# Kernel tuning notes

Measured on AMD Instinct MI355X. Metric: run time of the kernel, lower is better.

The kernel has to match this reference:

```python
import jax, jax.numpy as jnp
import numpy as np

# Model dims (Gemma-class)
B, T, HID = 1, 3072, 2048
H, KH, D = 16, 8, 128          # q heads, kv heads, head_dim
WIN = 1024                     # sliding window
EPS = 1e-6
SEQ = 1536                     # two packed sequences of length 1536


def _rms(x, w):
    # torch nn.RMSNorm: x * rsqrt(mean(x^2) + eps) [* weight]
    var = jnp.mean(x * x, axis=-1, keepdims=True)
    y = x * jax.lax.rsqrt(var + EPS)
    return y if w is None else y * w


def _rotate_half(x):
    x1, x2 = jnp.split(x, 2, axis=-1)
    return jnp.concatenate([-x2, x1], axis=-1)


def _rope(x, cos, sin):
    # x: [B,T,h,D]; cos/sin: [B,T,rd] -> unsqueeze head dim (matches cos.unsqueeze(2))
    c = cos[:, :, None, :]
    s = sin[:, :, None, :]
    rd = cos.shape[-1]
    xr, xp = x[..., :rd], x[..., rd:]
    xr = xr * c + _rotate_half(xr) * s
    return jnp.concatenate([xr, xp], axis=-1)


def _build_mask(cu_seqlens):
    # causal & within sliding window & same packed sequence (matches _sliding_mask)
    idx = jnp.arange(T)
    seg = jnp.searchsorted(cu_seqlens, idx, side='right') - 1
    i = idx[:, None]
    j = idx[None, :]
    return (i >= j) & ((i - j) < WIN) & (seg[:, None] == seg[None, :])


def _attn_layer(x, wq, qn, k, v, wo, cos, sin, mask):
    # x: [B,T,HID]; k,v: [T,KH,D] (possibly shared from an earlier layer)
    q = _rope(_rms((x @ wq).reshape(B, T, H, D), qn), cos, sin).reshape(T, H, D)
    rep = H // k.shape[1]
    kk = jnp.repeat(k, rep, axis=1)   # GQA: repeat_interleave over head dim
    vv = jnp.repeat(v, rep, axis=1)
    s = jnp.einsum('qhd,khd->hqk', q, kk)          # scale = 1.0 (as in source)
    s = jnp.where(mask, s, jnp.asarray(-1e30, s.dtype))
    p = jax.nn.softmax(s, axis=-1)
    o = jnp.einsum('hqk,khd->qhd', p, vv).reshape(B, T, H * D)
    return o @ wo


def setup_inputs() -> dict:
    key = jax.random.key(0)
    ks = jax.random.split(key, 10)
    hidden_states = jax.random.normal(ks[0], (B, T, HID), jnp.float32)
    # RoPE tables with per-packed-sequence position resets
    pos = jnp.concatenate([jnp.arange(SEQ), jnp.arange(SEQ)]).astype(jnp.float32)
    inv = 1.0 / (10000.0 ** (jnp.arange(0, D, 2, dtype=jnp.float32) / D))
    fr = pos[:, None] * inv[None, :]
    emb = jnp.concatenate([fr, fr], axis=-1)     # [T, D]
    cos = jnp.cos(emb)[None]                     # [1, T, D]
    sin = jnp.sin(emb)[None]
    w = lambda k, sh: 0.02 * jax.random.normal(k, sh, jnp.float32)
    return {
        'hidden_states': hidden_states,
        'cos': cos, 'sin': sin,
        'wq0': w(ks[1], (HID, H * D)), 'wk0': w(ks[2], (HID, KH * D)),
        'wv0': w(ks[3], (HID, KH * D)), 'wo0': w(ks[4], (H * D, HID)),
        'qn0': 1.0 + 0.01 * jax.random.normal(ks[5], (D,), jnp.float32),
        'kn0': 1.0 + 0.01 * jax.random.normal(ks[6], (D,), jnp.float32),
        'wq1': w(ks[7], (HID, H * D)), 'wo1': w(ks[8], (H * D, HID)),
        'qn1': 1.0 + 0.01 * jax.random.normal(ks[9], (D,), jnp.float32),
        'cu_seqlens': jnp.array([0, SEQ, T], dtype=jnp.int32),
    }


def reference(hidden_states, cos, sin, wq0, wk0, wv0, wo0, qn0, kn0, wq1, wo1, qn1, cu_seqlens):
    mask = _build_mask(cu_seqlens)
    # Layer 0: source layer -> computes and stores K/V
    k = _rope(_rms((hidden_states @ wk0).reshape(B, T, KH, D), kn0), cos, sin).reshape(T, KH, D)
    v = _rms((hidden_states @ wv0).reshape(B, T, KH, D), None).reshape(T, KH, D)
    out0 = _attn_layer(hidden_states, wq0, qn0, k, v, wo0, cos, sin, mask)
    # Layer 1: KV-shared layer -> reuses layer 0's K/V (skips k/v projections)
    out1 = _attn_layer(out0, wq1, qn1, k, v, wo1, cos, sin, mask)
    return out1
```

## Files before the change

kernel.cpp:

```cpp
#include <hip/hip_runtime.h>
#include <hip/hip_bf16.h>

#define T_TOK 3072
#define HIDDEN 2048
#define NHQ 16
#define NHKV 8
#define DH 128
#define WINDOW 1024

typedef __attribute__((ext_vector_type(4))) float f32x4;
typedef __attribute__((ext_vector_type(8))) short bf16x8;
typedef __attribute__((ext_vector_type(8))) unsigned short ushort8;
typedef __attribute__((ext_vector_type(4))) unsigned short ushort4v;

__device__ __forceinline__ unsigned short f2bf(float f) {
  union { float fv; unsigned u; } v; v.fv = f;
  unsigned r = v.u + 0x7fffu + ((v.u >> 16) & 1u);
  return (unsigned short)(r >> 16);
}
__device__ __forceinline__ float bf2f(unsigned short h) {
  union { unsigned u; float f; } v; v.u = ((unsigned)h) << 16;
  return v.f;
}
__device__ __forceinline__ void split2(float f, unsigned short& hi, unsigned short& lo) {
  hi = f2bf(f);
  lo = f2bf(f - bf2f(hi));
}

__global__ __launch_bounds__(256) void cvt_split(const float* __restrict__ x,
                                                 unsigned short* __restrict__ yh,
                                                 unsigned short* __restrict__ yl, int n) {
  int i = (blockIdx.x * 256 + threadIdx.x) * 4;
  if (i >= n) return;
  f32x4 v = *(const f32x4*)(x + i);
  ushort4v oh, ol;
#pragma unroll
  for (int j = 0; j < 4; ++j) {
    unsigned short h, l;
    split2(v[j], h, l);
    oh[j] = h; ol[j] = l;
  }
  *(ushort4v*)(yh + i) = oh;
  *(ushort4v*)(yl + i) = ol;
}

__global__ __launch_bounds__(256) void transpose_w_split(const float* __restrict__ W,
                                                         unsigned short* __restrict__ Wth,
                                                         unsigned short* __restrict__ Wtl,
                                                         int K, int N) {
  __shared__ float tile[32][33];
  int bn = blockIdx.x * 32, bk = blockIdx.y * 32;
  int tx = threadIdx.x & 31, ty = threadIdx.x >> 5;
#pragma unroll
  for (int i = 0; i < 4; ++i)
    tile[ty + i * 8][tx] = W[(size_t)(bk + ty + i * 8) * N + bn + tx];
  __syncthreads();
#pragma unroll
  for (int i = 0; i < 4; ++i) {
    unsigned short h, l;
    split2(tile[tx][ty + i * 8], h, l);
    Wth[(size_t)(bn + ty + i * 8) * K + bk + tx] = h;
    if (Wtl) Wtl[(size_t)(bn + ty + i * 8) * K + bk + tx] = l;
  }
}

__global__ __launch_bounds__(256) void transpose_u16(const unsigned short* __restrict__ src,
                                                     unsigned short* __restrict__ dst,
                                                     int R, int C) {
  __shared__ unsigned short tile[32][33];
  int bc = blockIdx.x * 32, br = blockIdx.y * 32;
  int tx = threadIdx.x & 31, ty = threadIdx.x >> 5;
#pragma unroll
  for (int i = 0; i < 4; ++i)
    tile[ty + i * 8][tx] = src[(size_t)(br + ty + i * 8) * C + bc + tx];
  __syncthreads();
#pragma unroll
  for (int i = 0; i < 4; ++i)
    dst[(size_t)(bc + ty + i * 8) * R + br + tx] = tile[tx][ty + i * 8];
}

template <int OUT>
__global__ __launch_bounds__(256) void gemm3(const unsigned short* __restrict__ Ah,
                                             const unsigned short* __restrict__ Al,
                                             const unsigned short* __restrict__ Bh,
                                             const unsigned short* __restrict__ Bl,
                                             float* __restrict__ Cf,
                                             unsigned short* __restrict__ Ch,
                                             unsigned short* __restrict__ Cl,
                                             int M, int N, int K) {
  __shared__ unsigned short ah_lds[128 * 32];
  __shared__ unsigned short al_lds[128 * 32];
  __shared__ unsigned short bh_lds[128 * 32];
  __shared__ unsigned short bl_lds[128 * 32];
  const int tid = threadIdx.x, lane = tid & 63, wave = tid >> 6;
  const int wr = (wave >> 1) * 64, wc = (wave & 1) * 64;
  const int g = lane >> 4, r16 = lane & 15;
  int nwg = gridDim.x * gridDim.y;
  int id = blockIdx.y * gridDim.x + blockIdx.x;
  int nid = (id & 7) * (nwg >> 3) + (id >> 3);
  const int bm = nid % gridDim.x, bn = nid / gridDim.x;
  f32x4 acc[4][4];
#pragma unroll
  for (int i = 0; i < 4; ++i)
#pragma unroll
    for (int j = 0; j < 4; ++j) acc[i][j] = (f32x4){0.f, 0.f, 0.f, 0.f};

  const unsigned short* AhB = Ah + (size_t)bm * 128 * K;
  const unsigned short* AlB = Al + (size_t)bm * 128 * K;
  const unsigned short* BhB = Bh + (size_t)bn * 128 * K;
  const unsigned short* BlB = Bl + (size_t)bn * 128 * K;

  for (int kt = 0; kt < K; kt += 32) {
    __syncthreads();
#pragma unroll
    for (int c = 0; c < 2; ++c) {
      size_t goff = (size_t)(wave * 32 + c * 16 + (lane >> 2)) * K + kt + (lane & 3) * 8;
      int loff = (wave * 2 + c) * 512;
      __builtin_amdgcn_global_load_lds(
          (const __attribute__((address_space(1))) unsigned int*)(AhB + goff),
          (__attribute__((address_space(3))) unsigned int*)(ah_lds + loff), 16, 0, 0);
      __builtin_amdgcn_global_load_lds(
          (const __attribute__((address_space(1))) unsigned int*)(AlB + goff),
          (__attribute__((address_space(3))) unsigned int*)(al_lds + loff), 16, 0, 0);
      __builtin_amdgcn_global_load_lds(
          (const __attribute__((address_space(1))) unsigned int*)(BhB + goff),
          (__attribute__((address_space(3))) unsigned int*)(bh_lds + loff), 16, 0, 0);
      __builtin_amdgcn_global_load_lds(
          (const __attribute__((address_space(1))) unsigned int*)(BlB + goff),
          (__attribute__((address_space(3))) unsigned int*)(bl_lds + loff), 16, 0, 0);
    }
    __syncthreads();
    bf16x8 ahf[4], alf[4], bhf[4], blf[4];
#pragma unroll
    for (int i = 0; i < 4; ++i) {
      ahf[i] = *(const bf16x8*)&ah_lds[(wr + i * 16 + r16) * 32 + g * 8];
      alf[i] = *(const bf16x8*)&al_lds[(wr + i * 16 + r16) * 32 + g * 8];
      bhf[i] = *(const bf16x8*)&bh_lds[(wc + i * 16 + r16) * 32 + g * 8];
      blf[i] = *(const bf16x8*)&bl_lds[(wc + i * 16 + r16) * 32 + g * 8];
    }
#pragma unroll
    for (int i = 0; i < 4; ++i)
#pragma unroll
      for (int j = 0; j < 4; ++j) {
        acc[i][j] = __builtin_amdgcn_mfma_f32_16x16x32_bf16(ahf[i], bhf[j], acc[i][j], 0, 0, 0);
        acc[i][j] = __builtin_amdgcn_mfma_f32_16x16x32_bf16(ahf[i], blf[j], acc[i][j], 0, 0, 0);
        acc[i][j] = __builtin_amdgcn_mfma_f32_16x16x32_bf16(alf[i], bhf[j], acc[i][j], 0, 0, 0);
      }
  }

#pragma unroll
  for (int i = 0; i < 4; ++i) {
    int row = bm * 128 + wr + i * 16 + g * 4;
#pragma unroll
    for (int j = 0; j < 4; ++j) {
      int col = bn * 128 + wc + j * 16 + r16;
#pragma unroll
      for (int r = 0; r < 4; ++r) {
        if (OUT == 0) {
          Cf[(size_t)(row + r) * N + col] = acc[i][j][r];
        } else {
          unsigned short h, l;
          split2(acc[i][j][r], h, l);
          Ch[(size_t)(row + r) * N + col] = h;
          Cl[(size_t)(row + r) * N + col] = l;
        }
      }
    }
  }
}

__global__ __launch_bounds__(256) void gemm1(const unsigned short* __restrict__ Ah,
                                             const unsigned short* __restrict__ Bh,
                                             float* __restrict__ Cf,
                                             int M, int N, int K) {
  __shared__ unsigned short ah_lds[128 * 32];
  __shared__ unsigned short bh_lds[128 * 32];
  const int tid = threadIdx.x, lane = tid & 63, wave = tid >> 6;
  const int wr = (wave >> 1) * 64, wc = (wave & 1) * 64;
  const int g = lane >> 4, r16 = lane & 15;
  int nwg = gridDim.x * gridDim.y;
  int id = blockIdx.y * gridDim.x + blockIdx.x;
  int nid = (id & 7) * (nwg >> 3) + (id >> 3);
  const int bm = nid % gridDim.x, bn = nid / gridDim.x;
  f32x4 acc[4][4];
#pragma unroll
  for (int i = 0; i < 4; ++i)
#pragma unroll
    for (int j = 0; j < 4; ++j) acc[i][j] = (f32x4){0.f, 0.f, 0.f, 0.f};

  const unsigned short* AhB = Ah + (size_t)bm * 128 * K;
  const unsigned short* BhB = Bh + (size_t)bn * 128 * K;

  for (int kt = 0; kt < K; kt += 32) {
    __syncthreads();
#pragma unroll
    for (int c = 0; c < 2; ++c) {
      size_t goff = (size_t)(wave * 32 + c * 16 + (lane >> 2)) * K + kt + (lane & 3) * 8;
      int loff = (wave * 2 + c) * 512;
      __builtin_amdgcn_global_load_lds(
          (const __attribute__((address_space(1))) unsigned int*)(AhB + goff),
          (__attribute__((address_space(3))) unsigned int*)(ah_lds + loff), 16, 0, 0);
      __builtin_amdgcn_global_load_lds(
          (const __attribute__((address_space(1))) unsigned int*)(BhB + goff),
          (__attribute__((address_space(3))) unsigned int*)(bh_lds + loff), 16, 0, 0);
    }
    __syncthreads();
    bf16x8 ahf[4], bhf[4];
#pragma unroll
    for (int i = 0; i < 4; ++i) {
      ahf[i] = *(const bf16x8*)&ah_lds[(wr + i * 16 + r16) * 32 + g * 8];
      bhf[i] = *(const bf16x8*)&bh_lds[(wc + i * 16 + r16) * 32 + g * 8];
    }
#pragma unroll
    for (int i = 0; i < 4; ++i)
#pragma unroll
      for (int j = 0; j < 4; ++j)
        acc[i][j] = __builtin_amdgcn_mfma_f32_16x16x32_bf16(ahf[i], bhf[j], acc[i][j], 0, 0, 0);
  }

#pragma unroll
  for (int i = 0; i < 4; ++i) {
    int row = bm * 128 + wr + i * 16 + g * 4;
#pragma unroll
    for (int j = 0; j < 4; ++j) {
      int col = bn * 128 + wc + j * 16 + r16;
#pragma unroll
      for (int r = 0; r < 4; ++r)
        Cf[(size_t)(row + r) * N + col] = acc[i][j][r];
    }
  }
}

__global__ __launch_bounds__(256) void rms_rope_split(const float* __restrict__ X,
                                                      const float* __restrict__ w,
                                                      const float* __restrict__ cosp,
                                                      const float* __restrict__ sinp,
                                                      unsigned short* __restrict__ outh,
                                                      unsigned short* __restrict__ outl,
                                                      int NH, int doRope) {
  int row = blockIdx.x * 4 + (threadIdx.x >> 6);
  int lane = threadIdx.x & 63;
  const float* x = X + (size_t)row * DH;
  float x1 = x[lane], x2 = x[lane + 64];
  float ss = x1 * x1 + x2 * x2;
#pragma unroll
  for (int m = 1; m < 64; m <<= 1) ss += __shfl_xor(ss, m, 64);
  float inv = rsqrtf(ss * (1.0f / 128.0f) + 1e-6f);
  float y1 = x1 * inv, y2 = x2 * inv;
  if (w) { y1 *= w[lane]; y2 *= w[lane + 64]; }
  if (doRope) {
    int t = row / NH;
    float c1 = cosp[t * DH + lane], s1 = sinp[t * DH + lane];
    float c2 = cosp[t * DH + lane + 64], s2 = sinp[t * DH + lane + 64];
    float o1 = y1 * c1 - y2 * s1;
    float o2 = y2 * c2 + y1 * s2;
    y1 = o1; y2 = o2;
  }
  unsigned short h, l;
  split2(y1, h, l);
  outh[(size_t)row * DH + lane] = h;
  if (outl) outl[(size_t)row * DH + lane] = l;
  split2(y2, h, l);
  outh[(size_t)row * DH + lane + 64] = h;
  if (outl) outl[(size_t)row * DH + lane + 64] = l;
}

template <int WRITE_LO>
__global__ __launch_bounds__(256) void attn3(const unsigned short* __restrict__ Qh,
                                             const unsigned short* __restrict__ Ql,
                                             const unsigned short* __restrict__ Kh,
                                             const unsigned short* __restrict__ Kl,
                                             const unsigned short* __restrict__ Vth,
                                             unsigned short* __restrict__ Oh,
                                             unsigned short* __restrict__ Ol,
                                             const int* __restrict__ cu, int ncu) {
  __shared__ unsigned short kh_lds[32][136];
  __shared__ unsigned short kl_lds[32][136];
  __shared__ unsigned short vh_lds[144][40];
  __shared__ unsigned short ph_lds[4][16][40];

  int id = blockIdx.y * gridDim.x + blockIdx.x;
  int nid = (id & 7) * 96 + (id >> 3);
  const int qt = nid % 48, h = nid / 48;
  const int qbase = qt * 64;
  const int kvh = h >> 1;
  const int tid = threadIdx.x, lane = tid & 63, wave = tid >> 6;
  const int g = lane >> 4, r16 = lane & 15;

  for (int i = tid; i < 16 * 40; i += 256) {
    int rr = i / 40, cc = i % 40;
    vh_lds[128 + rr][cc] = (rr == 0) ? (unsigned short)0x3F80 : (unsigned short)0;
  }

  bf16x8 aqh[4], aql[4];
  {
    const size_t qoff = ((size_t)(qbase + wave * 16 + r16) * NHQ + h) * DH;
#pragma unroll
    for (int ks = 0; ks < 4; ++ks) {
      aqh[ks] = *(const bf16x8*)(Qh + qoff + ks * 32 + g * 8);
      aql[ks] = *(const bf16x8*)(Ql + qoff + ks * 32 + g * 8);
    }
  }

  int ssr[4];
#pragma unroll
  for (int r = 0; r < 4; ++r) {
    int q_r = qbase + wave * 16 + g * 4 + r;
    int s = 0;
    for (int i = 1; i < ncu; ++i) { int v = cu[i]; if (v <= q_r) s = v; }
    ssr[r] = s;
  }
  int ss_base = 0;
  for (int i = 1; i < ncu; ++i) { int v = cu[i]; if (v <= qbase) ss_base = v; }

  float m_r[4] = {-1e30f, -1e30f, -1e30f, -1e30f};
  f32x4 oacc[8];
#pragma unroll
  for (int db = 0; db < 8; ++db) oacc[db] = (f32x4){0.f, 0.f, 0.f, 0.f};
  f32x4 oaccL = (f32x4){0.f, 0.f, 0.f, 0.f};

  int lo = qbase - WINDOW + 1;
  if (lo < ss_base) lo = ss_base;
  if (lo < 0) lo = 0;
  int kt0 = lo & ~31;
  int ktend = qbase + 63;

  const int krow = tid >> 3, kcol = (tid & 7) * 16;
  const int vd = tid >> 1, vhalf = (tid & 1) * 16;
  const int qmin = qbase + wave * 16;

  ushort8 rkh0, rkh1, rkl0, rkl1, rvh0, rvh1;
  auto loadTile = [&](int kt) {
    size_t goff = ((size_t)(kt + krow) * NHKV + kvh) * DH + kcol;
    rkh0 = *(const ushort8*)(Kh + goff);
    rkh1 = *(const ushort8*)(Kh + goff + 8);
    rkl0 = *(const ushort8*)(Kl + goff);
    rkl1 = *(const ushort8*)(Kl + goff + 8);
    size_t voff = ((size_t)kvh * DH + vd) * T_TOK + kt + vhalf;
    rvh0 = *(const ushort8*)(Vth + voff);
    rvh1 = *(const ushort8*)(Vth + voff + 8);
  };
  auto writeTile = [&]() {
    *(ushort8*)&kh_lds[krow][kcol] = rkh0;
    *(ushort8*)&kh_lds[krow][kcol + 8] = rkh1;
    *(ushort8*)&kl_lds[krow][kcol] = rkl0;
    *(ushort8*)&kl_lds[krow][kcol + 8] = rkl1;
    *(ushort8*)&vh_lds[vd][vhalf] = rvh0;
    *(ushort8*)&vh_lds[vd][vhalf + 8] = rvh1;
  };

  loadTile(kt0);
  writeTile();
  __syncthreads();

  for (int kt = kt0; kt <= ktend; kt += 32) {
    const bool hasNext = (kt + 32 <= ktend);
    if (hasNext) loadTile(kt + 32);

    f32x4 s0 = (f32x4){0.f, 0.f, 0.f, 0.f}, s1 = (f32x4){0.f, 0.f, 0.f, 0.f};
#pragma unroll
    for (int ks = 0; ks < 4; ++ks) {
      bf16x8 bh0 = *(const bf16x8*)&kh_lds[r16][ks * 32 + g * 8];
      bf16x8 bh1 = *(const bf16x8*)&kh_lds[16 + r16][ks * 32 + g * 8];
      bf16x8 bl0 = *(const bf16x8*)&kl_lds[r16][ks * 32 + g * 8];
      bf16x8 bl1 = *(const bf16x8*)&kl_lds[16 + r16][ks * 32 + g * 8];
      s0 = __builtin_amdgcn_mfma_f32_16x16x32_bf16(aqh[ks], bh0, s0, 0, 0, 0);
      s0 = __builtin_amdgcn_mfma_f32_16x16x32_bf16(aqh[ks], bl0, s0, 0, 0, 0);
      s0 = __builtin_amdgcn_mfma_f32_16x16x32_bf16(aql[ks], bh0, s0, 0, 0, 0);
      s1 = __builtin_amdgcn_mfma_f32_16x16x32_bf16(aqh[ks], bh1, s1, 0, 0, 0);
      s1 = __builtin_amdgcn_mfma_f32_16x16x32_bf16(aqh[ks], bl1, s1, 0, 0, 0);
      s1 = __builtin_amdgcn_mfma_f32_16x16x32_bf16(aql[ks], bh1, s1, 0, 0, 0);
    }

    float sv0_[4], sv1_[4], mt_[4];
    bool ok0_[4], ok1_[4];
    bool interior = (kt + 31 <= qmin) && (kt >= qmin + 16 - WINDOW) &&
                    __all(kt >= ssr[3]);
    if (interior) {
#pragma unroll
      for (int r = 0; r < 4; ++r) {
        ok0_[r] = ok1_[r] = true;
        sv0_[r] = s0[r]; sv1_[r] = s1[r];
      }
    } else {
#pragma unroll
      for (int r = 0; r < 4; ++r) {
        int q_r = qmin + g * 4 + r;
        int k0 = kt + r16, k1 = k0 + 16;
        ok0_[r] = (k0 <= q_r) && (k0 > q_r - WINDOW) && (k0 >= ssr[r]);
        ok1_[r] = (k1 <= q_r) && (k1 > q_r - WINDOW) && (k1 >= ssr[r]);
        sv0_[r] = ok0_[r] ? s0[r] : -1e30f;
        sv1_[r] = ok1_[r] ? s1[r] : -1e30f;
      }
    }
#pragma unroll
    for (int r = 0; r < 4; ++r) {
      float mt = fmaxf(sv0_[r], sv1_[r]);
#pragma unroll
      for (int mm = 1; mm < 16; mm <<= 1) mt = fmaxf(mt, __shfl_xor(mt, mm, 64));
      mt_[r] = mt;
    }
    float grow = fmaxf(fmaxf(mt_[0] - m_r[0], mt_[1] - m_r[1]),
                       fmaxf(mt_[2] - m_r[2], mt_[3] - m_r[3]));
    if (!__all(grow <= 8.0f)) {
#pragma unroll
      for (int r = 0; r < 4; ++r) {
        float mnew = fmaxf(m_r[r], mt_[r]);
        float alpha = __expf(m_r[r] - mnew);
        m_r[r] = mnew;
#pragma unroll
        for (int db = 0; db < 8; ++db) oacc[db][r] *= alpha;
        oaccL[r] *= alpha;
      }
    }
#pragma unroll
    for (int r = 0; r < 4; ++r) {
      float p0 = ok0_[r] ? __expf(sv0_[r] - m_r[r]) : 0.f;
      float p1 = ok1_[r] ? __expf(sv1_[r] - m_r[r]) : 0.f;
      ph_lds[wave][g * 4 + r][r16] = f2bf(p0);
      ph_lds[wave][g * 4 + r][16 + r16] = f2bf(p1);
    }

    bf16x8 pah = *(const bf16x8*)&ph_lds[wave][r16][g * 8];
#pragma unroll
    for (int db = 0; db < 8; ++db) {
      bf16x8 vfh = *(const bf16x8*)&vh_lds[db * 16 + r16][g * 8];
      oacc[db] = __builtin_amdgcn_mfma_f32_16x16x32_bf16(pah, vfh, oacc[db], 0, 0, 0);
    }
    {
      bf16x8 vfo = *(const bf16x8*)&vh_lds[128 + r16][g * 8];
      oaccL = __builtin_amdgcn_mfma_f32_16x16x32_bf16(pah, vfo, oaccL, 0, 0, 0);
    }

    __syncthreads();
    if (hasNext) writeTile();
    __syncthreads();
  }

#pragma unroll
  for (int r = 0; r < 4; ++r) {
    int q_r = qbase + wave * 16 + g * 4 + r;
    float lsum = __shfl(oaccL[r], lane & 48, 64);
    float invl = 1.f / lsum;
#pragma unroll
    for (int db = 0; db < 8; ++db) {
      float ov = oacc[db][r] * invl;
      unsigned short hh, ll;
      split2(ov, hh, ll);
      Oh[(size_t)q_r * (NHQ * DH) + h * DH + db * 16 + r16] = hh;
      if (WRITE_LO) Ol[(size_t)q_r * (NHQ * DH) + h * DH + db * 16 + r16] = ll;
    }
  }
}

extern "C" void kernel_launch(void* const* d_in, const int* in_sizes, int n_in,
                              void* d_out, int out_size, void* d_ws, size_t ws_size,
                              hipStream_t stream) {
  const float* hidden = (const float*)d_in[0];
  const float* cosp   = (const float*)d_in[1];
  const float* sinp   = (const float*)d_in[2];
  const float* wq0    = (const float*)d_in[3];
  const float* wk0    = (const float*)d_in[4];
  const float* wv0    = (const float*)d_in[5];
  const float* wo0    = (const float*)d_in[6];
  const float* qn0    = (const float*)d_in[7];
  const float* kn0    = (const float*)d_in[8];
  const float* wq1    = (const float*)d_in[9];
  const float* wo1    = (const float*)d_in[10];
  const float* qn1    = (const float*)d_in[11];
  const int*   cu     = (const int*)d_in[12];
  int ncu = in_sizes[12];

  char* p = (char*)d_ws;
  auto alloc = [&](size_t bytes) { char* r = p; p += (bytes + 255) & ~255ull; return r; };
  float*          c32  = (float*)alloc((size_t)T_TOK * HIDDEN * 4);
  unsigned short* xh   = (unsigned short*)alloc((size_t)T_TOK * HIDDEN * 2);
  unsigned short* xl   = (unsigned short*)alloc((size_t)T_TOK * HIDDEN * 2);
  unsigned short* wth  = (unsigned short*)alloc((size_t)HIDDEN * HIDDEN * 2);
  unsigned short* wtl  = (unsigned short*)alloc((size_t)HIDDEN * HIDDEN * 2);
  unsigned short* qh   = (unsigned short*)alloc((size_t)T_TOK * NHQ * DH * 2);
  unsigned short* ql   = (unsigned short*)alloc((size_t)T_TOK * NHQ * DH * 2);
  unsigned short* kh   = (unsigned short*)alloc((size_t)T_TOK * NHKV * DH * 2);
  unsigned short* kl   = (unsigned short*)alloc((size_t)T_TOK * NHKV * DH * 2);
  unsigned short* vh   = (unsigned short*)alloc((size_t)T_TOK * NHKV * DH * 2);
  unsigned short* vth  = (unsigned short*)alloc((size_t)T_TOK * NHKV * DH * 2);
  unsigned short* x1h  = (unsigned short*)alloc((size_t)T_TOK * HIDDEN * 2);
  unsigned short* x1l  = (unsigned short*)alloc((size_t)T_TOK * HIDDEN * 2);
  (void)ws_size; (void)n_in; (void)out_size;

  const int nX = T_TOK * HIDDEN;
  const int KVN = NHKV * DH;

  cvt_split<<<nX / 1024, 256, 0, stream>>>(hidden, xh, xl, nX);

  transpose_w_split<<<dim3(HIDDEN / 32, HIDDEN / 32), 256, 0, stream>>>(wq0, wth, wtl, HIDDEN, HIDDEN);
  gemm3<0><<<dim3(T_TOK / 128, HIDDEN / 128), 256, 0, stream>>>(xh, xl, wth, wtl, c32, nullptr, nullptr, T_TOK, HIDDEN, HIDDEN);
  rms_rope_split<<<T_TOK * NHQ / 4, 256, 0, stream>>>(c32, qn0, cosp, sinp, qh, ql, NHQ, 1);

  transpose_w_split<<<dim3(KVN / 32, HIDDEN / 32), 256, 0, stream>>>(wk0, wth, wtl, HIDDEN, KVN);
  gemm3<0><<<dim3(T_TOK / 128, KVN / 128), 256, 0, stream>>>(xh, xl, wth, wtl, c32, nullptr, nullptr, T_TOK, KVN, HIDDEN);
  rms_rope_split<<<T_TOK * NHKV / 4, 256, 0, stream>>>(c32, kn0, cosp, sinp, kh, kl, NHKV, 1);

  transpose_w_split<<<dim3(KVN / 32, HIDDEN / 32), 256, 0, stream>>>(wv0, wth, nullptr, HIDDEN, KVN);
  gemm1<<<dim3(T_TOK / 128, KVN / 128), 256, 0, stream>>>(xh, wth, c32, T_TOK, KVN, HIDDEN);
  rms_rope_split<<<T_TOK * NHKV / 4, 256, 0, stream>>>(c32, nullptr, cosp, sinp, vh, nullptr, NHKV, 0);

  transpose_u16<<<dim3(KVN / 32, T_TOK / 32), 256, 0, stream>>>(vh, vth, T_TOK, KVN);

  attn3<1><<<dim3(T_TOK / 64, NHQ), 256, 0, stream>>>(qh, ql, kh, kl, vth, xh, xl, cu, ncu);

  transpose_w_split<<<dim3(HIDDEN / 32, HIDDEN / 32), 256, 0, stream>>>(wo0, wth, wtl, HIDDEN, HIDDEN);
  gemm3<2><<<dim3(T_TOK / 128, HIDDEN / 128), 256, 0, stream>>>(xh, xl, wth, wtl, nullptr, x1h, x1l, T_TOK, HIDDEN, HIDDEN);

  transpose_w_split<<<dim3(HIDDEN / 32, HIDDEN / 32), 256, 0, stream>>>(wq1, wth, wtl, HIDDEN, HIDDEN);
  gemm3<0><<<dim3(T_TOK / 128, HIDDEN / 128), 256, 0, stream>>>(x1h, x1l, wth, wtl, c32, nullptr, nullptr, T_TOK, HIDDEN, HIDDEN);
  rms_rope_split<<<T_TOK * NHQ / 4, 256, 0, stream>>>(c32, qn1, cosp, sinp, qh, ql, NHQ, 1);

  attn3<0><<<dim3(T_TOK / 64, NHQ), 256, 0, stream>>>(qh, ql, kh, kl, vth, xh, nullptr, cu, ncu);

  transpose_w_split<<<dim3(HIDDEN / 32, HIDDEN / 32), 256, 0, stream>>>(wo1, wth, nullptr, HIDDEN, HIDDEN);
  gemm1<<<dim3(T_TOK / 128, HIDDEN / 128), 256, 0, stream>>>(xh, wth, (float*)d_out, T_TOK, HIDDEN, HIDDEN);
}
```

Measured before the change: 747.1 us.

## Load K/V MFMA operands directly from global memory instead of LDS staging

```diff
diff --git a/kernel.cpp b/kernel.cpp
--- a/kernel.cpp
+++ b/kernel.cpp
@@ -274,9 +274,6 @@
                                              unsigned short* __restrict__ Oh,
                                              unsigned short* __restrict__ Ol,
                                              const int* __restrict__ cu, int ncu) {
-  __shared__ unsigned short kh_lds[32][136];
-  __shared__ unsigned short kl_lds[32][136];
-  __shared__ unsigned short vh_lds[144][40];
   __shared__ unsigned short ph_lds[4][16][40];
 
   int id = blockIdx.y * gridDim.x + blockIdx.x;
@@ -287,11 +284,6 @@
   const int tid = threadIdx.x, lane = tid & 63, wave = tid >> 6;
   const int g = lane >> 4, r16 = lane & 15;
 
-  for (int i = tid; i < 16 * 40; i += 256) {
-    int rr = i / 40, cc = i % 40;
-    vh_lds[128 + rr][cc] = (rr == 0) ? (unsigned short)0x3F80 : (unsigned short)0;
-  }
-
   bf16x8 aqh[4], aql[4];
   {
     const size_t qoff = ((size_t)(qbase + wave * 16 + r16) * NHQ + h) * DH;
@@ -325,51 +317,41 @@
   int kt0 = lo & ~31;
   int ktend = qbase + 63;
 
-  const int krow = tid >> 3, kcol = (tid & 7) * 16;
-  const int vd = tid >> 1, vhalf = (tid & 1) * 16;
   const int qmin = qbase + wave * 16;
 
-  ushort8 rkh0, rkh1, rkl0, rkl1, rvh0, rvh1;
-  auto loadTile = [&](int kt) {
-    size_t goff = ((size_t)(kt + krow) * NHKV + kvh) * DH + kcol;
-    rkh0 = *(const ushort8*)(Kh + goff);
-    rkh1 = *(const ushort8*)(Kh + goff + 8);
-    rkl0 = *(const ushort8*)(Kl + goff);
-    rkl1 = *(const ushort8*)(Kl + goff + 8);
-    size_t voff = ((size_t)kvh * DH + vd) * T_TOK + kt + vhalf;
-    rvh0 = *(const ushort8*)(Vth + voff);
-    rvh1 = *(const ushort8*)(Vth + voff + 8);
-  };
-  auto writeTile = [&]() {
-    *(ushort8*)&kh_lds[krow][kcol] = rkh0;
-    *(ushort8*)&kh_lds[krow][kcol + 8] = rkh1;
-    *(ushort8*)&kl_lds[krow][kcol] = rkl0;
-    *(ushort8*)&kl_lds[krow][kcol + 8] = rkl1;
-    *(ushort8*)&vh_lds[vd][vhalf] = rvh0;
-    *(ushort8*)&vh_lds[vd][vhalf + 8] = rvh1;
-  };
-
-  loadTile(kt0);
-  writeTile();
-  __syncthreads();
+  bf16x8 vfo;
+#pragma unroll
+  for (int j = 0; j < 8; ++j) vfo[j] = (r16 == 0) ? (short)0x3F80 : (short)0;
+
+  const size_t kstr = (size_t)NHKV * DH;
+  const unsigned short* kh0 = Kh + ((size_t)r16 * NHKV + kvh) * DH + g * 8;
+  const unsigned short* kh1 = Kh + ((size_t)(r16 + 16) * NHKV + kvh) * DH + g * 8;
+  const unsigned short* kl0 = Kl + ((size_t)r16 * NHKV + kvh) * DH + g * 8;
+  const unsigned short* kl1 = Kl + ((size_t)(r16 + 16) * NHKV + kvh) * DH + g * 8;
+  const unsigned short* vt0 = Vth + ((size_t)(kvh * DH + r16)) * T_TOK + g * 8;
 
   for (int kt = kt0; kt <= ktend; kt += 32) {
-    const bool hasNext = (kt + 32 <= ktend);
-    if (hasNext) loadTile(kt + 32);
-
     f32x4 s0 = (f32x4){0.f, 0.f, 0.f, 0.f}, s1 = (f32x4){0.f, 0.f, 0.f, 0.f};
-#pragma unroll
-    for (int ks = 0; ks < 4; ++ks) {
-      bf16x8 bh0 = *(const bf16x8*)&kh_lds[r16][ks * 32 + g * 8];
-      bf16x8 bh1 = *(const bf16x8*)&kh_lds[16 + r16][ks * 32 + g * 8];
-      bf16x8 bl0 = *(const bf16x8*)&kl_lds[r16][ks * 32 + g * 8];
-      bf16x8 bl1 = *(const bf16x8*)&kl_lds[16 + r16][ks * 32 + g * 8];
-      s0 = __builtin_amdgcn_mfma_f32_16x16x32_bf16(aqh[ks], bh0, s0, 0, 0, 0);
-      s0 = __builtin_amdgcn_mfma_f32_16x16x32_bf16(aqh[ks], bl0, s0, 0, 0, 0);
-      s0 = __builtin_amdgcn_mfma_f32_16x16x32_bf16(aql[ks], bh0, s0, 0, 0, 0);
-      s1 = __builtin_amdgcn_mfma_f32_16x16x32_bf16(aqh[ks], bh1, s1, 0, 0, 0);
-      s1 = __builtin_amdgcn_mfma_f32_16x16x32_bf16(aqh[ks], bl1, s1, 0, 0, 0);
-      s1 = __builtin_amdgcn_mfma_f32_16x16x32_bf16(aql[ks], bh1, s1, 0, 0, 0);
+    {
+      const unsigned short* p0 = kh0 + (size_t)kt * kstr;
+      const unsigned short* p1 = kh1 + (size_t)kt * kstr;
+      const unsigned short* q0 = kl0 + (size_t)kt * kstr;
+      const unsigned short* q1 = kl1 + (size_t)kt * kstr;
+      __builtin_amdgcn_s_setprio(1);
+#pragma unroll
+      for (int ks = 0; ks < 4; ++ks) {
+        bf16x8 bh0 = *(const bf16x8*)(p0 + ks * 32);
+        bf16x8 bh1 = *(const bf16x8*)(p1 + ks * 32);
+        bf16x8 bl0 = *(const bf16x8*)(q0 + ks * 32);
+        bf16x8 bl1 = *(const bf16x8*)(q1 + ks * 32);
+        s0 = __builtin_amdgcn_mfma_f32_16x16x32_bf16(aqh[ks], bh0, s0, 0, 0, 0);
+        s0 = __builtin_amdgcn_mfma_f32_16x16x32_bf16(aqh[ks], bl0, s0, 0, 0, 0);
+        s0 = __builtin_amdgcn_mfma_f32_16x16x32_bf16(aql[ks], bh0, s0, 0, 0, 0);
+        s1 = __builtin_amdgcn_mfma_f32_16x16x32_bf16(aqh[ks], bh1, s1, 0, 0, 0);
+        s1 = __builtin_amdgcn_mfma_f32_16x16x32_bf16(aqh[ks], bl1, s1, 0, 0, 0);
+        s1 = __builtin_amdgcn_mfma_f32_16x16x32_bf16(aql[ks], bh1, s1, 0, 0, 0);
+      }
+      __builtin_amdgcn_s_setprio(0);
     }
 
     float sv0_[4], sv1_[4], mt_[4];
@@ -415,26 +397,24 @@
     }
 #pragma unroll
     for (int r = 0; r < 4; ++r) {
-      float p0 = ok0_[r] ? __expf(sv0_[r] - m_r[r]) : 0.f;
-      float p1 = ok1_[r] ? __expf(sv1_[r] - m_r[r]) : 0.f;
-      ph_lds[wave][g * 4 + r][r16] = f2bf(p0);
-      ph_lds[wave][g * 4 + r][16 + r16] = f2bf(p1);
+      float p0v = ok0_[r] ? __expf(sv0_[r] - m_r[r]) : 0.f;
+      float p1v = ok1_[r] ? __expf(sv1_[r] - m_r[r]) : 0.f;
+      ph_lds[wave][g * 4 + r][r16] = f2bf(p0v);
+      ph_lds[wave][g * 4 + r][16 + r16] = f2bf(p1v);
     }
 
     bf16x8 pah = *(const bf16x8*)&ph_lds[wave][r16][g * 8];
-#pragma unroll
-    for (int db = 0; db < 8; ++db) {
-      bf16x8 vfh = *(const bf16x8*)&vh_lds[db * 16 + r16][g * 8];
-      oacc[db] = __builtin_amdgcn_mfma_f32_16x16x32_bf16(pah, vfh, oacc[db], 0, 0, 0);
-    }
     {
-      bf16x8 vfo = *(const bf16x8*)&vh_lds[128 + r16][g * 8];
+      const unsigned short* vb = vt0 + kt;
+      __builtin_amdgcn_s_setprio(1);
+#pragma unroll
+      for (int db = 0; db < 8; ++db) {
+        bf16x8 vfh = *(const bf16x8*)(vb + (size_t)db * 16 * T_TOK);
+        oacc[db] = __builtin_amdgcn_mfma_f32_16x16x32_bf16(pah, vfh, oacc[db], 0, 0, 0);
+      }
       oaccL = __builtin_amdgcn_mfma_f32_16x16x32_bf16(pah, vfo, oaccL, 0, 0, 0);
-    }
-
-    __syncthreads();
-    if (hasNext) writeTile();
-    __syncthreads();
+      __builtin_amdgcn_s_setprio(0);
+    }
   }
 
 #pragma unroll
```

Result: slower. 979.3 us (+31.1%).

## Halve GEMM M-tile to 64 and fuse K/V projections into one GEMM

Applied to the files above, without the earlier changes.

```diff
diff --git a/kernel.cpp b/kernel.cpp
--- a/kernel.cpp
+++ b/kernel.cpp
@@ -80,48 +80,52 @@
 }
 
 template <int OUT>
-__global__ __launch_bounds__(256) void gemm3(const unsigned short* __restrict__ Ah,
-                                             const unsigned short* __restrict__ Al,
-                                             const unsigned short* __restrict__ Bh,
-                                             const unsigned short* __restrict__ Bl,
-                                             float* __restrict__ Cf,
-                                             unsigned short* __restrict__ Ch,
-                                             unsigned short* __restrict__ Cl,
-                                             int M, int N, int K) {
-  __shared__ unsigned short ah_lds[128 * 32];
-  __shared__ unsigned short al_lds[128 * 32];
+__global__ __launch_bounds__(256) void gemm3_64(const unsigned short* __restrict__ Ah,
+                                                const unsigned short* __restrict__ Al,
+                                                const unsigned short* __restrict__ Bh,
+                                                const unsigned short* __restrict__ Bl,
+                                                float* __restrict__ Cf,
+                                                unsigned short* __restrict__ Ch,
+                                                unsigned short* __restrict__ Cl,
+                                                int M, int N, int K) {
+  __shared__ unsigned short ah_lds[64 * 32];
+  __shared__ unsigned short al_lds[64 * 32];
   __shared__ unsigned short bh_lds[128 * 32];
   __shared__ unsigned short bl_lds[128 * 32];
   const int tid = threadIdx.x, lane = tid & 63, wave = tid >> 6;
-  const int wr = (wave >> 1) * 64, wc = (wave & 1) * 64;
+  const int wr = (wave >> 1) * 32, wc = (wave & 1) * 64;
   const int g = lane >> 4, r16 = lane & 15;
   int nwg = gridDim.x * gridDim.y;
   int id = blockIdx.y * gridDim.x + blockIdx.x;
   int nid = (id & 7) * (nwg >> 3) + (id >> 3);
   const int bm = nid % gridDim.x, bn = nid / gridDim.x;
-  f32x4 acc[4][4];
-#pragma unroll
-  for (int i = 0; i < 4; ++i)
+  f32x4 acc[2][4];
+#pragma unroll
+  for (int i = 0; i < 2; ++i)
 #pragma unroll
     for (int j = 0; j < 4; ++j) acc[i][j] = (f32x4){0.f, 0.f, 0.f, 0.f};
 
-  const unsigned short* AhB = Ah + (size_t)bm * 128 * K;
-  const unsigned short* AlB = Al + (size_t)bm * 128 * K;
+  const unsigned short* AhB = Ah + (size_t)bm * 64 * K;
+  const unsigned short* AlB = Al + (size_t)bm * 64 * K;
   const unsigned short* BhB = Bh + (size_t)bn * 128 * K;
   const unsigned short* BlB = Bl + (size_t)bn * 128 * K;
 
   for (int kt = 0; kt < K; kt += 32) {
     __syncthreads();
-#pragma unroll
-    for (int c = 0; c < 2; ++c) {
-      size_t goff = (size_t)(wave * 32 + c * 16 + (lane >> 2)) * K + kt + (lane & 3) * 8;
-      int loff = (wave * 2 + c) * 512;
+    {
+      size_t goff = (size_t)(wave * 16 + (lane >> 2)) * K + kt + (lane & 3) * 8;
+      int loff = wave * 512;
       __builtin_amdgcn_global_load_lds(
           (const __attribute__((address_space(1))) unsigned int*)(AhB + goff),
           (__attribute__((address_space(3))) unsigned int*)(ah_lds + loff), 16, 0, 0);
       __builtin_amdgcn_global_load_lds(
           (const __attribute__((address_space(1))) unsigned int*)(AlB + goff),
           (__attribute__((address_space(3))) unsigned int*)(al_lds + loff), 16, 0, 0);
+    }
+#pragma unroll
+    for (int c = 0; c < 2; ++c) {
+      size_t goff = (size_t)(wave * 32 + c * 16 + (lane >> 2)) * K + kt + (lane & 3) * 8;
+      int loff = (wave * 2 + c) * 512;
       __builtin_amdgcn_global_load_lds(
           (const __attribute__((address_space(1))) unsigned int*)(BhB + goff),
           (__attribute__((address_space(3))) unsigned int*)(bh_lds + loff), 16, 0, 0);
@@ -130,16 +134,19 @@
           (__attribute__((address_space(3))) unsigned int*)(bl_lds + loff), 16, 0, 0);
     }
     __syncthreads();
-    bf16x8 ahf[4], alf[4], bhf[4], blf[4];
-#pragma unroll
-    for (int i = 0; i < 4; ++i) {
+    bf16x8 ahf[2], alf[2], bhf[4], blf[4];
+#pragma unroll
+    for (int i = 0; i < 2; ++i) {
       ahf[i] = *(const bf16x8*)&ah_lds[(wr + i * 16 + r16) * 32 + g * 8];
       alf[i] = *(const bf16x8*)&al_lds[(wr + i * 16 + r16) * 32 + g * 8];
-      bhf[i] = *(const bf16x8*)&bh_lds[(wc + i * 16 + r16) * 32 + g * 8];
-      blf[i] = *(const bf16x8*)&bl_lds[(wc + i * 16 + r16) * 32 + g * 8];
-    }
-#pragma unroll
-    for (int i = 0; i < 4; ++i)
+    }
+#pragma unroll
+    for (int j = 0; j < 4; ++j) {
+      bhf[j] = *(const bf16x8*)&bh_lds[(wc + j * 16 + r16) * 32 + g * 8];
+      blf[j] = *(const bf16x8*)&bl_lds[(wc + j * 16 + r16) * 32 + g * 8];
+    }
+#pragma unroll
+    for (int i = 0; i < 2; ++i)
 #pragma unroll
       for (int j = 0; j < 4; ++j) {
         acc[i][j] = __builtin_amdgcn_mfma_f32_16x16x32_bf16(ahf[i], bhf[j], acc[i][j], 0, 0, 0);
@@ -149,8 +156,8 @@
   }
 
 #pragma unroll
-  for (int i = 0; i < 4; ++i) {
-    int row = bm * 128 + wr + i * 16 + g * 4;
+  for (int i = 0; i < 2; ++i) {
+    int row = bm * 64 + wr + i * 16 + g * 4;
 #pragma unroll
     for (int j = 0; j < 4; ++j) {
       int col = bn * 128 + wc + j * 16 + r16;
@@ -169,58 +176,61 @@
   }
 }
 
-__global__ __launch_bounds__(256) void gemm1(const unsigned short* __restrict__ Ah,
-                                             const unsigned short* __restrict__ Bh,
-                                             float* __restrict__ Cf,
-                                             int M, int N, int K) {
-  __shared__ unsigned short ah_lds[128 * 32];
+__global__ __launch_bounds__(256) void gemm1_64(const unsigned short* __restrict__ Ah,
+                                                const unsigned short* __restrict__ Bh,
+                                                float* __restrict__ Cf,
+                                                int M, int N, int K) {
+  __shared__ unsigned short ah_lds[64 * 32];
   __shared__ unsigned short bh_lds[128 * 32];
   const int tid = threadIdx.x, lane = tid & 63, wave = tid >> 6;
-  const int wr = (wave >> 1) * 64, wc = (wave & 1) * 64;
+  const int wr = (wave >> 1) * 32, wc = (wave & 1) * 64;
   const int g = lane >> 4, r16 = lane & 15;
   int nwg = gridDim.x * gridDim.y;
   int id = blockIdx.y * gridDim.x + blockIdx.x;
   int nid = (id & 7) * (nwg >> 3) + (id >> 3);
   const int bm = nid % gridDim.x, bn = nid / gridDim.x;
-  f32x4 acc[4][4];
-#pragma unroll
-  for (int i = 0; i < 4; ++i)
+  f32x4 acc[2][4];
+#pragma unroll
+  for (int i = 0; i < 2; ++i)
 #pragma unroll
     for (int j = 0; j < 4; ++j) acc[i][j] = (f32x4){0.f, 0.f, 0.f, 0.f};
 
-  const unsigned short* AhB = Ah + (size_t)bm * 128 * K;
+  const unsigned short* AhB = Ah + (size_t)bm * 64 * K;
   const unsigned short* BhB = Bh + (size_t)bn * 128 * K;
 
   for (int kt = 0; kt < K; kt += 32) {
     __syncthreads();
+    {
+      size_t goff = (size_t)(wave * 16 + (lane >> 2)) * K + kt + (lane & 3) * 8;
+      __builtin_amdgcn_global_load_lds(
+          (const __attribute__((address_space(1))) unsigned int*)(AhB + goff),
+          (__attribute__((address_space(3))) unsigned int*)(ah_lds + wave * 512), 16, 0, 0);
+    }
 #pragma unroll
     for (int c = 0; c < 2; ++c) {
       size_t goff = (size_t)(wave * 32 + c * 16 + (lane >> 2)) * K + kt + (lane & 3) * 8;
-      int loff = (wave * 2 + c) * 512;
-      __builtin_amdgcn_global_load_lds(
-          (const __attribute__((address_space(1))) unsigned int*)(AhB + goff),
-          (__attribute__((address_space(3))) unsigned int*)(ah_lds + loff), 16, 0, 0);
       __builtin_amdgcn_global_load_lds(
           (const __attribute__((address_space(1))) unsigned int*)(BhB + goff),
-          (__attribute__((address_space(3))) unsigned int*)(bh_lds + loff), 16, 0, 0);
+          (__attribute__((address_space(3))) unsigned int*)(bh_lds + (wave * 2 + c) * 512), 16, 0, 0);
     }
     __syncthreads();
-    bf16x8 ahf[4], bhf[4];
-#pragma unroll
-    for (int i = 0; i < 4; ++i) {
+    bf16x8 ahf[2], bhf[4];
+#pragma unroll
+    for (int i = 0; i < 2; ++i)
       ahf[i] = *(const bf16x8*)&ah_lds[(wr + i * 16 + r16) * 32 + g * 8];
-      bhf[i] = *(const bf16x8*)&bh_lds[(wc + i * 16 + r16) * 32 + g * 8];
-    }
-#pragma unroll
-    for (int i = 0; i < 4; ++i)
+#pragma unroll
+    for (int j = 0; j < 4; ++j)
+      bhf[j] = *(const bf16x8*)&bh_lds[(wc + j * 16 + r16) * 32 + g * 8];
+#pragma unroll
+    for (int i = 0; i < 2; ++i)
 #pragma unroll
       for (int j = 0; j < 4; ++j)
         acc[i][j] = __builtin_amdgcn_mfma_f32_16x16x32_bf16(ahf[i], bhf[j], acc[i][j], 0, 0, 0);
   }
 
 #pragma unroll
-  for (int i = 0; i < 4; ++i) {
-    int row = bm * 128 + wr + i * 16 + g * 4;
+  for (int i = 0; i < 2; ++i) {
+    int row = bm * 64 + wr + i * 16 + g * 4;
 #pragma unroll
     for (int j = 0; j < 4; ++j) {
       int col = bn * 128 + wc + j * 16 + r16;
@@ -237,10 +247,11 @@
                                                       const float* __restrict__ sinp,
                                                       unsigned short* __restrict__ outh,
                                                       unsigned short* __restrict__ outl,
-                                                      int NH, int doRope) {
+                                                      int NH, int doRope, int XS, int XO) {
   int row = blockIdx.x * 4 + (threadIdx.x >> 6);
   int lane = threadIdx.x & 63;
-  const float* x = X + (size_t)row * DH;
+  int t = row / NH, hh_ = row % NH;
+  const float* x = X + (size_t)t * XS + XO + (size_t)hh_ * DH;
   float x1 = x[lane], x2 = x[lane + 64];
   float ss = x1 * x1 + x2 * x2;
 #pragma unroll
@@ -249,7 +260,6 @@
   float y1 = x1 * inv, y2 = x2 * inv;
   if (w) { y1 *= w[lane]; y2 *= w[lane + 64]; }
   if (doRope) {
-    int t = row / NH;
     float c1 = cosp[t * DH + lane], s1 = sinp[t * DH + lane];
     float c2 = cosp[t * DH + lane + 64], s2 = sinp[t * DH + lane + 64];
     float o1 = y1 * c1 - y2 * s1;
@@ -277,7 +287,7 @@
   __shared__ unsigned short kh_lds[32][136];
   __shared__ unsigned short kl_lds[32][136];
   __shared__ unsigned short vh_lds[144][40];
-  __shared__ unsigned short ph_lds[4][16][40];
+  __shared__ unsigned short ph_lds[4][16][44];
 
   int id = blockIdx.y * gridDim.x + blockIdx.x;
   int nid = (id & 7) * 96 + (id >> 3);
@@ -415,10 +425,10 @@
     }
 #pragma unroll
     for (int r = 0; r < 4; ++r) {
-      float p0 = ok0_[r] ? __expf(sv0_[r] - m_r[r]) : 0.f;
-      float p1 = ok1_[r] ? __expf(sv1_[r] - m_r[r]) : 0.f;
-      ph_lds[wave][g * 4 + r][r16] = f2bf(p0);
-      ph_lds[wave][g * 4 + r][16 + r16] = f2bf(p1);
+      float p0v = ok0_[r] ? __expf(sv0_[r] - m_r[r]) : 0.f;
+      float p1v = ok1_[r] ? __expf(sv1_[r] - m_r[r]) : 0.f;
+      ph_lds[wave][g * 4 + r][r16] = f2bf(p0v);
+      ph_lds[wave][g * 4 + r][16 + r16] = f2bf(p1v);
     }
 
     bf16x8 pah = *(const bf16x8*)&ph_lds[wave][r16][g * 8];
@@ -494,30 +504,29 @@
   cvt_split<<<nX / 1024, 256, 0, stream>>>(hidden, xh, xl, nX);
 
   transpose_w_split<<<dim3(HIDDEN / 32, HIDDEN / 32), 256, 0, stream>>>(wq0, wth, wtl, HIDDEN, HIDDEN);
-  gemm3<0><<<dim3(T_TOK / 128, HIDDEN / 128), 256, 0, stream>>>(xh, xl, wth, wtl, c32, nullptr, nullptr, T_TOK, HIDDEN, HIDDEN);
-  rms_rope_split<<<T_TOK * NHQ / 4, 256, 0, stream>>>(c32, qn0, cosp, sinp, qh, ql, NHQ, 1);
+  gemm3_64<0><<<dim3(T_TOK / 64, HIDDEN / 128), 256, 0, stream>>>(xh, xl, wth, wtl, c32, nullptr, nullptr, T_TOK, HIDDEN, HIDDEN);
+  rms_rope_split<<<T_TOK * NHQ / 4, 256, 0, stream>>>(c32, qn0, cosp, sinp, qh, ql, NHQ, 1, HIDDEN, 0);
 
   transpose_w_split<<<dim3(KVN / 32, HIDDEN / 32), 256, 0, stream>>>(wk0, wth, wtl, HIDDEN, KVN);
-  gemm3<0><<<dim3(T_TOK / 128, KVN / 128), 256, 0, stream>>>(xh, xl, wth, wtl, c32, nullptr, nullptr, T_TOK, KVN, HIDDEN);
-  rms_rope_split<<<T_TOK * NHKV / 4, 256, 0, stream>>>(c32, kn0, cosp, sinp, kh, kl, NHKV, 1);
-
-  transpose_w_split<<<dim3(KVN / 32, HIDDEN / 32), 256, 0, stream>>>(wv0, wth, nullptr, HIDDEN, KVN);
-  gemm1<<<dim3(T_TOK / 128, KVN / 128), 256, 0, stream>>>(xh, wth, c32, T_TOK, KVN, HIDDEN);
-  rms_rope_split<<<T_TOK * NHKV / 4, 256, 0, stream>>>(c32, nullptr, cosp, sinp, vh, nullptr, NHKV, 0);
+  transpose_w_split<<<dim3(KVN / 32, HIDDEN / 32), 256, 0, stream>>>(
+      wv0, wth + (size_t)KVN * HIDDEN, wtl + (size_t)KVN * HIDDEN, HIDDEN, KVN);
+  gemm3_64<0><<<dim3(T_TOK / 64, (2 * KVN) / 128), 256, 0, stream>>>(xh, xl, wth, wtl, c32, nullptr, nullptr, T_TOK, 2 * KVN, HIDDEN);
+  rms_rope_split<<<T_TOK * NHKV / 4, 256, 0, stream>>>(c32, kn0, cosp, sinp, kh, kl, NHKV, 1, 2 * KVN, 0);
+  rms_rope_split<<<T_TOK * NHKV / 4, 256, 0, stream>>>(c32, nullptr, cosp, sinp, vh, nullptr, NHKV, 0, 2 * KVN, KVN);
 
   transpose_u16<<<dim3(KVN / 32, T_TOK / 32), 256, 0, stream>>>(vh, vth, T_TOK, KVN);
 
   attn3<1><<<dim3(T_TOK / 64, NHQ), 256, 0, stream>>>(qh, ql, kh, kl, vth, xh, xl, cu, ncu);
 
   transpose_w_split<<<dim3(HIDDEN / 32, HIDDEN / 32), 256, 0, stream>>>(wo0, wth, wtl, HIDDEN, HIDDEN);
-  gemm3<2><<<dim3(T_TOK / 128, HIDDEN / 128), 256, 0, stream>>>(xh, xl, wth, wtl, nullptr, x1h, x1l, T_TOK, HIDDEN, HIDDEN);
+  gemm3_64<2><<<dim3(T_TOK / 64, HIDDEN / 128), 256, 0, stream>>>(xh, xl, wth, wtl, nullptr, x1h, x1l, T_TOK, HIDDEN, HIDDEN);
 
   transpose_w_split<<<dim3(HIDDEN / 32, HIDDEN / 32), 256, 0, stream>>>(wq1, wth, wtl, HIDDEN, HIDDEN);
-  gemm3<0><<<dim3(T_TOK / 128, HIDDEN / 128), 256, 0, stream>>>(x1h, x1l, wth, wtl, c32, nullptr, nullptr, T_TOK, HIDDEN, HIDDEN);
-  rms_rope_split<<<T_TOK * NHQ / 4, 256, 0, stream>>>(c32, qn1, cosp, sinp, qh, ql, NHQ, 1);
+  gemm3_64<0><<<dim3(T_TOK / 64, HIDDEN / 128), 256, 0, stream>>>(x1h, x1l, wth, wtl, c32, nullptr, nullptr, T_TOK, HIDDEN, HIDDEN);
+  rms_rope_split<<<T_TOK * NHQ / 4, 256, 0, stream>>>(c32, qn1, cosp, sinp, qh, ql, NHQ, 1, HIDDEN, 0);
 
   attn3<0><<<dim3(T_TOK / 64, NHQ), 256, 0, stream>>>(qh, ql, kh, kl, vth, xh, nullptr, cu, ncu);
 
   transpose_w_split<<<dim3(HIDDEN / 32, HIDDEN / 32), 256, 0, stream>>>(wo1, wth, nullptr, HIDDEN, HIDDEN);
-  gemm1<<<dim3(T_TOK / 128, HIDDEN / 128), 256, 0, stream>>>(xh, wth, (float*)d_out, T_TOK, HIDDEN, HIDDEN);
-}
+  gemm1_64<<<dim3(T_TOK / 64, HIDDEN / 128), 256, 0, stream>>>(xh, wth, (float*)d_out, T_TOK, HIDDEN, HIDDEN);
+}
```

New measurement: 753.7 us. Within noise of the previous version (+0.9%).
